# Performance work log

Hardware: AMD Instinct MI355X
Metric: run time of the kernel (lower is better)

Reference implementation:

```python
import jax, jax.numpy as jnp
import numpy as np

G = 512  # number of graphs per batch


def gcn_conv(x, edge_index, edge_attr, W):
    # x:[N,Fin], edge_index:[2,E], edge_attr:[E,1], W:[Fin,Fout]
    n = x.shape[0]
    loop = jnp.arange(n)
    row = jnp.concatenate([edge_index[0], loop])
    col = jnp.concatenate([edge_index[1], loop])
    w = jnp.concatenate([edge_attr[:, 0], jnp.ones((n,), x.dtype)])
    deg = jnp.zeros((n,), x.dtype).at[col].add(jnp.ones_like(w))
    dinv = jnp.clip(deg, 1e-12) ** -0.5
    norm = dinv[row] * w * dinv[col]
    h = x @ W  # [N,Fout]
    msg = h[row] * norm[:, None]  # [E+N,Fout] gather+scale
    return jnp.zeros_like(h).at[col].add(msg)  # scatter-add


def mean_pool(x, batch):
    s = jnp.zeros((G, x.shape[1]), x.dtype).at[batch].add(x)
    c = jnp.zeros((G,), x.dtype).at[batch].add(1.0)
    return s / jnp.clip(c, 1.0)[:, None]


def setup_inputs() -> dict:
    key = jax.random.key(0)
    ks = jax.random.split(key, 32)
    Nd, Ed, Np, Ep = 100000, 500000, 200000, 2000000
    d = {
        "drug_x": jax.random.normal(ks[0], (Nd, 78), jnp.float32),
        "drug_edge_index": jax.random.randint(ks[1], (2, Ed), 0, Nd),
        "drug_edge_attr": jax.random.uniform(ks[2], (Ed, 1), jnp.float32),
        "drug_batch": jnp.sort(jax.random.randint(ks[3], (Nd,), 0, G)),
        "protein_x": jax.random.normal(ks[4], (Np, 20), jnp.float32),
        "protein_edge_index": jax.random.randint(ks[5], (2, Ep), 0, Np),
        "protein_edge_attr": jax.random.uniform(ks[6], (Ep, 1), jnp.float32),
        "protein_batch": jnp.sort(jax.random.randint(ks[7], (Np,), 0, G)),
    }
    def w(k, i, o):
        return jax.random.normal(k, (i, o), jnp.float32) / np.sqrt(i)
    d.update({
        "dW1": w(ks[8], 78, 78), "dW2": w(ks[9], 78, 156), "dW3": w(ks[10], 156, 312),
        "dL1_w": w(ks[11], 312, 1024), "dL1_b": jnp.zeros((1024,), jnp.float32),
        "dL2_w": w(ks[12], 1024, 64), "dL2_b": jnp.zeros((64,), jnp.float32),
        "pW1": w(ks[13], 20, 20), "pW2": w(ks[14], 20, 40), "pW3": w(ks[15], 40, 80),
        "pL1_w": w(ks[16], 80, 1024), "pL1_b": jnp.zeros((1024,), jnp.float32),
        "pL2_w": w(ks[17], 1024, 64), "pL2_b": jnp.zeros((64,), jnp.float32),
        "fW1": w(ks[18], 128, 1024), "fb1": jnp.zeros((1024,), jnp.float32),
        "fW2": w(ks[19], 1024, 512), "fb2": jnp.zeros((512,), jnp.float32),
        "fW3": w(ks[20], 512, 1), "fb3": jnp.zeros((1,), jnp.float32),
    })
    return d


def reference(drug_x, drug_edge_index, drug_edge_attr, drug_batch,
              protein_x, protein_edge_index, protein_edge_attr, protein_batch,
              dW1, dW2, dW3, dL1_w, dL1_b, dL2_w, dL2_b,
              pW1, pW2, pW3, pL1_w, pL1_b, pL2_w, pL2_b,
              fW1, fb1, fW2, fb2, fW3, fb3):
    relu = jax.nn.relu
    x = relu(gcn_conv(drug_x, drug_edge_index, drug_edge_attr, dW1))
    x = relu(gcn_conv(x, drug_edge_index, drug_edge_attr, dW2))
    x = relu(gcn_conv(x, drug_edge_index, drug_edge_attr, dW3))
    x = mean_pool(x, drug_batch)
    x = relu(x @ dL1_w + dL1_b)
    x = relu(x @ dL2_w + dL2_b)
    p = relu(gcn_conv(protein_x, protein_edge_index, protein_edge_attr, pW1))
    p = relu(gcn_conv(p, protein_edge_index, protein_edge_attr, pW2))
    p = relu(gcn_conv(p, protein_edge_index, protein_edge_attr, pW3))
    p = mean_pool(p, protein_batch)
    p = relu(p @ pL1_w + pL1_b)
    p = relu(p @ pL2_w + pL2_b)
    c = jnp.concatenate([x, p], axis=1)  # [G,128]
    h = relu(c @ fW1 + fb1)
    h = relu(h @ fW2 + fb2)
    out = h @ fW3 + fb3  # [G,1]
    return out[:, 0]
```

## Files before the change

kernel.cpp:

```cpp
#include <hip/hip_runtime.h>
#include <math.h>

#define NGRAPH 512

typedef __attribute__((ext_vector_type(8))) __bf16 bf16x8;
typedef __attribute__((ext_vector_type(4))) float f32x4;

__device__ __forceinline__ unsigned short f2bf(float x) {
    unsigned int u = __float_as_uint(x);
    u = (u + 0x7fffu + ((u >> 16) & 1u)) >> 16;
    return (unsigned short)u;
}
__device__ __forceinline__ float bf2f(unsigned short b) {
    return __uint_as_float(((unsigned int)b) << 16);
}

static inline unsigned grid_for(size_t n, int block = 256) {
    return (unsigned)((n + block - 1) / block);
}

__global__ void fill_i32(int* __restrict__ p, int v, size_t n) {
    size_t i = blockIdx.x * (size_t)blockDim.x + threadIdx.x;
    if (i < n) p[i] = v;
}

__global__ void fill_f32(float* __restrict__ p, float v, size_t n) {
    size_t i = blockIdx.x * (size_t)blockDim.x + threadIdx.x;
    if (i < n) p[i] = v;
}

__global__ void hist_kernel(const int* __restrict__ col, int E, int* __restrict__ cnt) {
    size_t i = blockIdx.x * (size_t)blockDim.x + threadIdx.x;
    if (i < (size_t)E) atomicAdd(&cnt[col[i]], 1);
}

__global__ void wcvt_t(const float* __restrict__ in, unsigned short* __restrict__ out,
                       int K, int N, int KPAD) {
    int i = blockIdx.x * blockDim.x + threadIdx.x;
    if (i >= N * KPAD) return;
    int n = i / KPAD, k = i - n * KPAD;
    out[i] = (k < K) ? f2bf(in[(size_t)k * N + n]) : (unsigned short)0;
}

__global__ void scan_pass1(const int* __restrict__ in, int* __restrict__ bsum,
                           float* __restrict__ dinv, int n) {
    __shared__ int sdata[256];
    int tid = threadIdx.x;
    int i = blockIdx.x * 256 + tid;
    int v = (i < n) ? in[i] : 0;
    if (i < n) dinv[i] = 1.0f / sqrtf((float)v + 1.0f);
    sdata[tid] = v;
    __syncthreads();
    for (int s = 128; s > 0; s >>= 1) {
        if (tid < s) sdata[tid] += sdata[tid + s];
        __syncthreads();
    }
    if (tid == 0) bsum[blockIdx.x] = sdata[0];
}

__global__ void scan_pass2(int* __restrict__ bsum, int nb) {
    __shared__ int s[1024];
    int tid = threadIdx.x;
    int v = (tid < nb) ? bsum[tid] : 0;
    s[tid] = v;
    __syncthreads();
    for (int ofs = 1; ofs < 1024; ofs <<= 1) {
        int t = (tid >= ofs) ? s[tid - ofs] : 0;
        __syncthreads();
        s[tid] += t;
        __syncthreads();
    }
    if (tid < nb) bsum[tid] = s[tid] - v;
}

__global__ void scan_pass3(int* __restrict__ pos, const int* __restrict__ bsum, int n) {
    __shared__ int sdata[256];
    int tid = threadIdx.x;
    int i = blockIdx.x * 256 + tid;
    int v = (i < n) ? pos[i] : 0;
    sdata[tid] = v;
    __syncthreads();
    for (int ofs = 1; ofs < 256; ofs <<= 1) {
        int t = (tid >= ofs) ? sdata[tid - ofs] : 0;
        __syncthreads();
        sdata[tid] += t;
        __syncthreads();
    }
    if (i < n) pos[i] = sdata[tid] - v + bsum[blockIdx.x];
}

__global__ void csr_fill(const int* __restrict__ row, const int* __restrict__ col,
                         const float* __restrict__ attr, const float* __restrict__ dinv,
                         int* __restrict__ pos, int2* __restrict__ rcp, int E) {
    size_t i = blockIdx.x * (size_t)blockDim.x + threadIdx.x;
    if (i >= (size_t)E) return;
    int r = row[i], c = col[i];
    int slot = atomicAdd(&pos[c], 1);
    rcp[slot] = make_int2(r, __float_as_int(dinv[r] * attr[i] * dinv[c]));
}

template <int V, int LPG, int F, int LDI, int LDO, bool INBF>
__global__ void gather_bf(const int* __restrict__ pos, const int2* __restrict__ rcp,
                          const void* __restrict__ Xv, const float* __restrict__ dinv,
                          unsigned short* __restrict__ AGG, int N) {
    constexpr int gpb = 256 / LPG;
    int grp = threadIdx.x / LPG;
    if (grp >= gpb) return;
    int gid = blockIdx.x * gpb + grp;
    int lane = threadIdx.x - grp * LPG;
    if (gid >= N) return;

    auto load_row = [&](int r, float* dst) {
        if (INBF) {
            const unsigned short* X = (const unsigned short*)Xv;
            if (V == 2) {
                unsigned int u = *reinterpret_cast<const unsigned int*>(X + (size_t)r * LDI + lane * 2);
                dst[0] = bf2f((unsigned short)(u & 0xffffu));
                dst[1] = bf2f((unsigned short)(u >> 16));
            } else {
                uint2 u = *reinterpret_cast<const uint2*>(X + (size_t)r * LDI + lane * 4);
                dst[0] = bf2f((unsigned short)(u.x & 0xffffu));
                dst[1] = bf2f((unsigned short)(u.x >> 16));
                dst[2] = bf2f((unsigned short)(u.y & 0xffffu));
                dst[3] = bf2f((unsigned short)(u.y >> 16));
            }
        } else {
            const float* X = (const float*)Xv;
            if (V == 2) {
                float2 u = *reinterpret_cast<const float2*>(X + (size_t)r * LDI + lane * 2);
                dst[0] = u.x; dst[1] = u.y;
            } else {
                float4 u = *reinterpret_cast<const float4*>(X + (size_t)r * LDI + lane * 4);
                dst[0] = u.x; dst[1] = u.y; dst[2] = u.z; dst[3] = u.w;
            }
        }
    };

    int start = (gid == 0) ? 0 : pos[gid - 1];
    int end = pos[gid];
    float s = dinv[gid];
    float s2 = s * s;
    float acc[V];
    load_row(gid, acc);
#pragma unroll
    for (int j = 0; j < V; ++j) acc[j] *= s2;
    int t = start;
    for (; t + 4 <= end; t += 4) {
        int2 e0 = rcp[t], e1 = rcp[t + 1], e2 = rcp[t + 2], e3 = rcp[t + 3];
        float c0 = __int_as_float(e0.y), c1 = __int_as_float(e1.y);
        float c2 = __int_as_float(e2.y), c3 = __int_as_float(e3.y);
        float h0[V], h1[V], h2[V], h3[V];
        load_row(e0.x, h0); load_row(e1.x, h1); load_row(e2.x, h2); load_row(e3.x, h3);
#pragma unroll
        for (int j = 0; j < V; ++j) {
            float v = fmaf(c0, h0[j], acc[j]);
            v = fmaf(c1, h1[j], v);
            v = fmaf(c2, h2[j], v);
            acc[j] = fmaf(c3, h3[j], v);
        }
    }
    for (; t < end; ++t) {
        int2 e = rcp[t];
        float cf = __int_as_float(e.y);
        float h[V];
        load_row(e.x, h);
#pragma unroll
        for (int j = 0; j < V; ++j) acc[j] = fmaf(cf, h[j], acc[j]);
    }
    unsigned short* op = AGG + (size_t)gid * LDO + lane * V;
    if (V == 2) {
        unsigned int p = (unsigned int)f2bf(acc[0]) | ((unsigned int)f2bf(acc[1]) << 16);
        *reinterpret_cast<unsigned int*>(op) = p;
    } else {
        uint2 p;
        p.x = (unsigned int)f2bf(acc[0]) | ((unsigned int)f2bf(acc[1]) << 16);
        p.y = (unsigned int)f2bf(acc[2]) | ((unsigned int)f2bf(acc[3]) << 16);
        *reinterpret_cast<uint2*>(op) = p;
    }
    constexpr int PAD = LDO - F;
#pragma unroll
    for (int p = lane; p < PAD; p += LPG) AGG[(size_t)gid * LDO + F + p] = 0;
}

template <int KPAD, int BN>
__global__ __launch_bounds__(256) void tgemm_mfma(
        const unsigned short* __restrict__ A, const unsigned short* __restrict__ Wt,
        unsigned short* __restrict__ C, int M, int N, int ldc) {
    constexpr int CH = KPAD / 8;
    constexpr int KSTEPS = KPAD / 32;
    constexpr int NI = (BN / 2) / 16;
    __shared__ unsigned short As[128 * KPAD];
    const int tid = threadIdx.x;
    const int m0 = blockIdx.y * 128;
    const int n0 = blockIdx.x * BN;

    for (int idx = tid; idx < 128 * CH; idx += 256) {
        int m = idx / CH;
        int c = idx - m * CH;
        int gm = m0 + m;
        uint4 v = make_uint4(0u, 0u, 0u, 0u);
        if (gm < M) v = *reinterpret_cast<const uint4*>(A + (size_t)gm * KPAD + c * 8);
        int cs = c ^ (m & 7);
        *reinterpret_cast<uint4*>(&As[m * KPAD + cs * 8]) = v;
    }
    __syncthreads();

    const int wid = tid >> 6;
    const int l = tid & 63;
    const int wm = wid >> 1, wn = wid & 1;
    const int lr = l & 15, lg = l >> 4;

    f32x4 acc[4][NI];
#pragma unroll
    for (int i = 0; i < 4; ++i)
#pragma unroll
        for (int j = 0; j < NI; ++j) acc[i][j] = (f32x4){0.f, 0.f, 0.f, 0.f};

    for (int ks = 0; ks < KSTEPS; ++ks) {
        bf16x8 a[4], b[NI];
#pragma unroll
        for (int mi = 0; mi < 4; ++mi) {
            int row = wm * 64 + mi * 16 + lr;
            int cs = (ks * 4 + lg) ^ (row & 7);
            a[mi] = *reinterpret_cast<const bf16x8*>(&As[row * KPAD + cs * 8]);
        }
#pragma unroll
        for (int ni = 0; ni < NI; ++ni) {
            int gn = n0 + wn * (BN / 2) + ni * 16 + lr;
            int gns = (gn < N) ? gn : (N - 1);
            b[ni] = *reinterpret_cast<const bf16x8*>(
                &Wt[(size_t)gns * KPAD + ks * 32 + lg * 8]);
        }
#pragma unroll
        for (int mi = 0; mi < 4; ++mi)
#pragma unroll
            for (int ni = 0; ni < NI; ++ni)
                acc[mi][ni] = __builtin_amdgcn_mfma_f32_16x16x32_bf16(
                    a[mi], b[ni], acc[mi][ni], 0, 0, 0);
    }

#pragma unroll
    for (int mi = 0; mi < 4; ++mi) {
#pragma unroll
        for (int ni = 0; ni < NI; ++ni) {
#pragma unroll
            for (int j = 0; j < 4; ++j) {
                int gm = m0 + wm * 64 + mi * 16 + lg * 4 + j;
                int gn = n0 + wn * (BN / 2) + ni * 16 + lr;
                if (gm < M && gn < N)
                    C[(size_t)gm * ldc + gn] = f2bf(fmaxf(acc[mi][ni][j], 0.0f));
            }
        }
    }
}

template <int F2, int SUB>
__global__ void pool_part_bf(const unsigned short* __restrict__ X, const int* __restrict__ batch,
                             float* __restrict__ pool, int N, int PB) {
    int g = blockIdx.x / PB;
    int st = blockIdx.x - g * PB;
    int tid = threadIdx.x;
    int p = tid % F2;
    int sub = tid / F2;
    if (sub >= SUB) return;
    int lo = 0, hi = N;
    while (lo < hi) { int mid = (lo + hi) >> 1; if (batch[mid] < g) lo = mid + 1; else hi = mid; }
    int s0 = lo;
    hi = N;
    while (lo < hi) { int mid = (lo + hi) >> 1; if (batch[mid] < g + 1) lo = mid + 1; else hi = mid; }
    int s1 = lo;
    const int F = 2 * F2;
    int stride = PB * SUB;
    float a0 = 0.0f, a1 = 0.0f;
    for (int n = s0 + st * SUB + sub; n < s1; n += stride) {
        unsigned int u = *reinterpret_cast<const unsigned int*>(X + (size_t)n * F + 2 * p);
        a0 += fmaxf(bf2f((unsigned short)(u & 0xffffu)), 0.0f);
        a1 += fmaxf(bf2f((unsigned short)(u >> 16)), 0.0f);
    }
    atomicAdd(&pool[(size_t)g * F + 2 * p], a0);
    atomicAdd(&pool[(size_t)g * F + 2 * p + 1], a1);
}

__global__ void pool_div_g(float* __restrict__ pool, const int* __restrict__ batch,
                           int N, int F) {
    int g = blockIdx.x;
    int lo = 0, hi = N;
    while (lo < hi) { int mid = (lo + hi) >> 1; if (batch[mid] < g) lo = mid + 1; else hi = mid; }
    int s0 = lo;
    hi = N;
    while (lo < hi) { int mid = (lo + hi) >> 1; if (batch[mid] < g + 1) lo = mid + 1; else hi = mid; }
    int c = lo - s0;
    float inv = 1.0f / (float)(c > 0 ? c : 1);
    for (int f = threadIdx.x; f < F; f += blockDim.x)
        pool[(size_t)g * F + f] *= inv;
}

template <int K, int NOUT, bool INBF>
__global__ __launch_bounds__(64 * (K / 4)) void fused_conv_bf(
        const int* __restrict__ pos, const int2* __restrict__ rcp,
        const void* __restrict__ Xv, const float* __restrict__ dinv,
        const float* __restrict__ W, unsigned short* __restrict__ Y, int N) {
    constexpr int LPG = K / 4;
    constexpr int NTHREADS = 64 * LPG;
    __shared__ float Ws[K][NOUT];
    __shared__ float Ag[64][K + 8];
    const int tid = threadIdx.x;
    const int nid0 = blockIdx.x * 64;

    for (int i = tid; i < K * NOUT; i += NTHREADS) Ws[i / NOUT][i % NOUT] = W[i];

    int grp = tid / LPG, lane = tid % LPG;
    int gid = nid0 + grp;

    auto load_row = [&](int r, float* dst) {
        if (INBF) {
            const unsigned short* X = (const unsigned short*)Xv;
            uint2 u = *reinterpret_cast<const uint2*>(X + (size_t)r * K + lane * 4);
            dst[0] = bf2f((unsigned short)(u.x & 0xffffu));
            dst[1] = bf2f((unsigned short)(u.x >> 16));
            dst[2] = bf2f((unsigned short)(u.y & 0xffffu));
            dst[3] = bf2f((unsigned short)(u.y >> 16));
        } else {
            const float* X = (const float*)Xv;
            float4 u = *reinterpret_cast<const float4*>(X + (size_t)r * K + lane * 4);
            dst[0] = u.x; dst[1] = u.y; dst[2] = u.z; dst[3] = u.w;
        }
    };

    if (gid < N) {
        int start = (gid == 0) ? 0 : pos[gid - 1];
        int end = pos[gid];
        float s = dinv[gid];
        float s2 = s * s;
        float acc[4];
        load_row(gid, acc);
#pragma unroll
        for (int j = 0; j < 4; ++j) acc[j] *= s2;
        int t = start;
        for (; t + 4 <= end; t += 4) {
            int2 e0 = rcp[t], e1 = rcp[t + 1], e2 = rcp[t + 2], e3 = rcp[t + 3];
            float c0 = __int_as_float(e0.y), c1 = __int_as_float(e1.y);
            float c2 = __int_as_float(e2.y), c3 = __int_as_float(e3.y);
            float h0[4], h1[4], h2[4], h3[4];
            load_row(e0.x, h0); load_row(e1.x, h1); load_row(e2.x, h2); load_row(e3.x, h3);
#pragma unroll
            for (int j = 0; j < 4; ++j) {
                float v = fmaf(c0, h0[j], acc[j]);
                v = fmaf(c1, h1[j], v);
                v = fmaf(c2, h2[j], v);
                acc[j] = fmaf(c3, h3[j], v);
            }
        }
        for (; t < end; ++t) {
            int2 e = rcp[t];
            float cf = __int_as_float(e.y);
            float h[4];
            load_row(e.x, h);
#pragma unroll
            for (int j = 0; j < 4; ++j) acc[j] = fmaf(cf, h[j], acc[j]);
        }
#pragma unroll
        for (int j = 0; j < 4; ++j) Ag[grp][lane * 4 + j] = acc[j];
    }
    __syncthreads();

    for (int idx = tid; idx < 64 * NOUT; idx += NTHREADS) {
        int nl = idx / NOUT, n = idx % NOUT;
        int g = nid0 + nl;
        if (g < N) {
            float acc = 0.0f;
#pragma unroll
            for (int k = 0; k < K; ++k) acc = fmaf(Ag[nl][k], Ws[k][n], acc);
            Y[(size_t)g * NOUT + n] = f2bf(fmaxf(acc, 0.0f));
        }
    }
}

template <bool RELU_OUT>
__global__ __launch_bounds__(256) void skinny_gemm4(
        const float* __restrict__ A, const float* __restrict__ W,
        const float* __restrict__ bias, float* __restrict__ C,
        int K, int M, int ldc, int coff) {
    __shared__ float As[4][1024];
    __shared__ float red[4][64][4];
    const int tid = threadIdx.x;
    const int m_l = tid & 63;
    const int q = tid >> 6;
    const int g0 = blockIdx.y * 4;
    const int m0 = blockIdx.x * 64;

    for (int idx = tid; idx < 4 * K; idx += 256)
        As[idx / K][idx % K] = A[(size_t)(g0 + idx / K) * K + idx % K];
    __syncthreads();

    const int Kq = (K + 3) >> 2;
    const int ks = q * Kq;
    const int ke = (ks + Kq < K) ? ks + Kq : K;
    const int m = m0 + m_l;
    float acc[4] = {0.0f, 0.0f, 0.0f, 0.0f};
    if (m < M) {
        for (int k = ks; k < ke; ++k) {
            float w = W[(size_t)k * M + m];
            acc[0] = fmaf(As[0][k], w, acc[0]);
            acc[1] = fmaf(As[1][k], w, acc[1]);
            acc[2] = fmaf(As[2][k], w, acc[2]);
            acc[3] = fmaf(As[3][k], w, acc[3]);
        }
    }
#pragma unroll
    for (int g = 0; g < 4; ++g) red[q][m_l][g] = acc[g];
    __syncthreads();
    if (q == 0 && m < M) {
        float b = bias[m];
#pragma unroll
        for (int g = 0; g < 4; ++g) {
            float v = red[0][m_l][g] + red[1][m_l][g] + red[2][m_l][g] + red[3][m_l][g] + b;
            if (RELU_OUT) v = fmaxf(v, 0.0f);
            C[(size_t)(g0 + g) * ldc + coff + m] = v;
        }
    }
}

__global__ void final_kernel(const float* __restrict__ A, const float* __restrict__ w,
                             const float* __restrict__ b, float* __restrict__ out, int K) {
    int wave = (blockIdx.x * blockDim.x + threadIdx.x) >> 6;
    int lane = threadIdx.x & 63;
    if (wave >= NGRAPH) return;
    const float* ar = A + (size_t)wave * K;
    float acc = 0.0f;
    for (int k = lane; k < K; k += 64) acc = fmaf(ar[k], w[k], acc);
#pragma unroll
    for (int s = 32; s > 0; s >>= 1) acc += __shfl_down(acc, s, 64);
    if (lane == 0) out[wave] = acc + b[0];
}

static void build_csr(const int* row, const int* col, const float* attr,
                      int N, int E, float* dinv, int* pos,
                      int2* rcp, int* bsum, hipStream_t stream) {
    const int B = 256;
    int nb = (N + 255) / 256;
    fill_i32<<<grid_for(N), B, 0, stream>>>(pos, 0, (size_t)N);
    hist_kernel<<<grid_for(E), B, 0, stream>>>(col, E, pos);
    scan_pass1<<<nb, B, 0, stream>>>(pos, bsum, dinv, N);
    scan_pass2<<<1, 1024, 0, stream>>>(bsum, nb);
    scan_pass3<<<nb, B, 0, stream>>>(pos, bsum, N);
    csr_fill<<<grid_for(E), B, 0, stream>>>(row, col, attr, dinv, pos, rcp, E);
}

extern "C" void kernel_launch(void* const* d_in, const int* in_sizes, int n_in,
                              void* d_out, int out_size, void* d_ws, size_t ws_size,
                              hipStream_t stream) {
    const float* drug_x  = (const float*)d_in[0];
    const int*   d_ei    = (const int*)d_in[1];
    const float* d_ea    = (const float*)d_in[2];
    const int*   d_batch = (const int*)d_in[3];
    const float* prot_x  = (const float*)d_in[4];
    const int*   p_ei    = (const int*)d_in[5];
    const float* p_ea    = (const float*)d_in[6];
    const int*   p_batch = (const int*)d_in[7];
    const float* dW1 = (const float*)d_in[8];
    const float* dW2 = (const float*)d_in[9];
    const float* dW3 = (const float*)d_in[10];
    const float* dL1_w = (const float*)d_in[11];
    const float* dL1_b = (const float*)d_in[12];
    const float* dL2_w = (const float*)d_in[13];
    const float* dL2_b = (const float*)d_in[14];
    const float* pW1 = (const float*)d_in[15];
    const float* pW2 = (const float*)d_in[16];
    const float* pW3 = (const float*)d_in[17];
    const float* pL1_w = (const float*)d_in[18];
    const float* pL1_b = (const float*)d_in[19];
    const float* pL2_w = (const float*)d_in[20];
    const float* pL2_b = (const float*)d_in[21];
    const float* fW1 = (const float*)d_in[22];
    const float* fb1 = (const float*)d_in[23];
    const float* fW2 = (const float*)d_in[24];
    const float* fb2 = (const float*)d_in[25];
    const float* fW3 = (const float*)d_in[26];
    const float* fb3 = (const float*)d_in[27];
    float* out = (float*)d_out;

    const int Nd = in_sizes[0] / 78;
    const int Ed = in_sizes[1] / 2;
    const int Np = in_sizes[4] / 20;
    const int Ep = in_sizes[5] / 2;
    const int* d_row = d_ei;
    const int* d_col = d_ei + Ed;
    const int* p_row = p_ei;
    const int* p_col = p_ei + Ep;

    float* ws = (float*)d_ws;
    size_t off = 0;
    auto align256 = [](size_t n) -> size_t { return (n + 255) & ~(size_t)255; };
    auto take = [&](size_t n) -> float* {
        float* p = ws + off;
        off += align256(n);
        return p;
    };
    float* B1      = take((size_t)Nd * 312);
    float* B2      = take((size_t)Nd * 312);
    float* dinv_d  = take((size_t)Nd);
    float* dinv_p  = take((size_t)Np);
    float* pool    = take((size_t)NGRAPH * 312);
    float* t1      = take((size_t)NGRAPH * 1024);
    float* Cbuf    = take((size_t)NGRAPH * 128);
    float* f2buf   = take((size_t)NGRAPH * 512);
    int*   bsum    = (int*)take(1056);
    int*   pos_d   = (int*)take((size_t)Nd);
    int2*  rcp_d   = (int2*)take((size_t)Ed * 2);
    unsigned short* Wt1 = (unsigned short*)take((78 * 128) / 2);
    unsigned short* Wt2 = (unsigned short*)take((156 * 128) / 2);
    unsigned short* Wt3 = (unsigned short*)take((312 * 192) / 2);
    size_t tail = align256((size_t)Np * 80);
    int*   pos_p   = (int*)(B1 + tail);
    int2*  rcp_p   = (int2*)(B1 + tail + align256((size_t)Np));
    (void)ws_size;

    unsigned short* B1u = (unsigned short*)B1;
    unsigned short* B2u = (unsigned short*)B2;

    const int B = 256;
    auto gblocks = [](int n, int gpb) -> unsigned { return (unsigned)((n + gpb - 1) / gpb); };
    auto mgrid = [](int M, int N, int BN) -> dim3 {
        return dim3((unsigned)((N + BN - 1) / BN), (unsigned)((M + 127) / 128));
    };

    build_csr(d_row, d_col, d_ea, Nd, Ed, dinv_d, pos_d, rcp_d, bsum, stream);
    wcvt_t<<<grid_for(78 * 128), B, 0, stream>>>(dW1, Wt1, 78, 78, 128);
    wcvt_t<<<grid_for(156 * 128), B, 0, stream>>>(dW2, Wt2, 78, 156, 128);
    wcvt_t<<<grid_for(312 * 192), B, 0, stream>>>(dW3, Wt3, 156, 312, 192);

    gather_bf<2, 39, 78, 78, 128, false><<<gblocks(Nd, 256 / 39), B, 0, stream>>>(
        pos_d, rcp_d, drug_x, dinv_d, B2u, Nd);
    tgemm_mfma<128, 64><<<mgrid(Nd, 78, 64), B, 0, stream>>>(B2u, Wt1, B1u, Nd, 78, 80);

    gather_bf<2, 39, 78, 80, 128, true><<<gblocks(Nd, 256 / 39), B, 0, stream>>>(
        pos_d, rcp_d, B1u, dinv_d, B2u, Nd);
    tgemm_mfma<128, 64><<<mgrid(Nd, 156, 64), B, 0, stream>>>(B2u, Wt2, B1u, Nd, 156, 156);

    gather_bf<4, 39, 156, 156, 192, true><<<gblocks(Nd, 256 / 39), B, 0, stream>>>(
        pos_d, rcp_d, B1u, dinv_d, B2u, Nd);
    tgemm_mfma<192, 64><<<mgrid(Nd, 312, 64), B, 0, stream>>>(B2u, Wt3, B1u, Nd, 312, 312);

    fill_f32<<<grid_for((size_t)NGRAPH * 312), B, 0, stream>>>(pool, 0.0f, (size_t)NGRAPH * 312);
    pool_part_bf<156, 1><<<NGRAPH * 8, B, 0, stream>>>(B1u, d_batch, pool, Nd, 8);
    pool_div_g<<<NGRAPH, B, 0, stream>>>(pool, d_batch, Nd, 312);

    skinny_gemm4<true><<<dim3(16, NGRAPH / 4), B, 0, stream>>>(pool, dL1_w, dL1_b, t1, 312, 1024, 1024, 0);
    skinny_gemm4<true><<<dim3(1, NGRAPH / 4), B, 0, stream>>>(t1, dL2_w, dL2_b, Cbuf, 1024, 64, 128, 0);

    build_csr(p_row, p_col, p_ea, Np, Ep, dinv_p, pos_p, rcp_p, bsum, stream);

    fused_conv_bf<20, 20, false><<<gblocks(Np, 64), 320, 0, stream>>>(
        pos_p, rcp_p, prot_x, dinv_p, pW1, B1u, Np);
    fused_conv_bf<20, 40, true><<<gblocks(Np, 64), 320, 0, stream>>>(
        pos_p, rcp_p, B1u, dinv_p, pW2, B2u, Np);
    fused_conv_bf<40, 80, true><<<gblocks(Np, 64), 640, 0, stream>>>(
        pos_p, rcp_p, B2u, dinv_p, pW3, B1u, Np);

    fill_f32<<<grid_for((size_t)NGRAPH * 80), B, 0, stream>>>(pool, 0.0f, (size_t)NGRAPH * 80);
    pool_part_bf<40, 6><<<NGRAPH * 8, B, 0, stream>>>(B1u, p_batch, pool, Np, 8);
    pool_div_g<<<NGRAPH, B, 0, stream>>>(pool, p_batch, Np, 80);

    skinny_gemm4<true><<<dim3(16, NGRAPH / 4), B, 0, stream>>>(pool, pL1_w, pL1_b, t1, 80, 1024, 1024, 0);
    skinny_gemm4<true><<<dim3(1, NGRAPH / 4), B, 0, stream>>>(t1, pL2_w, pL2_b, Cbuf, 1024, 64, 128, 64);

    skinny_gemm4<true><<<dim3(16, NGRAPH / 4), B, 0, stream>>>(Cbuf, fW1, fb1, t1, 128, 1024, 1024, 0);
    skinny_gemm4<true><<<dim3(8, NGRAPH / 4), B, 0, stream>>>(t1, fW2, fb2, f2buf, 1024, 512, 512, 0);
    final_kernel<<<grid_for((size_t)NGRAPH * 64), B, 0, stream>>>(f2buf, fW3, fb3, out, 512);
}
```

Measured before the change: 1.024 ms.

## Build CSR via two-level binning to localize atomics in shared memory

Result: slower. 1.563 ms (+52.7%).

```diff
diff --git a/kernel.cpp b/kernel.cpp
--- a/kernel.cpp
+++ b/kernel.cpp
@@ -87,16 +87,42 @@
         __syncthreads();
     }
     if (i < n) pos[i] = sdata[tid] - v + bsum[blockIdx.x];
-}
-
-__global__ void csr_fill(const int* __restrict__ row, const int* __restrict__ col,
+    if (i == n - 1) pos[n] = sdata[tid] + bsum[blockIdx.x];
+}
+
+__global__ void bump_init(const int* __restrict__ pos, int* __restrict__ bump, int NB, int SPB) {
+    int b = blockIdx.x * blockDim.x + threadIdx.x;
+    if (b < NB) bump[b] = pos[b * SPB];
+}
+
+__global__ void bin_fill(const int* __restrict__ row, const int* __restrict__ col,
                          const float* __restrict__ attr, const float* __restrict__ dinv,
-                         int* __restrict__ pos, int2* __restrict__ rcp, int E) {
+                         int* __restrict__ bump, int4* __restrict__ tmp, int E, int SPB) {
     size_t i = blockIdx.x * (size_t)blockDim.x + threadIdx.x;
     if (i >= (size_t)E) return;
     int r = row[i], c = col[i];
-    int slot = atomicAdd(&pos[c], 1);
-    rcp[slot] = make_int2(r, __float_as_int(dinv[r] * attr[i] * dinv[c]));
+    int slot = atomicAdd(&bump[c / SPB], 1);
+    tmp[slot] = make_int4(r, c, __float_as_int(dinv[r] * attr[i] * dinv[c]), 0);
+}
+
+template <int SPB>
+__global__ __launch_bounds__(256) void csr_place(const int* __restrict__ pos,
+                                                 const int4* __restrict__ tmp,
+                                                 int2* __restrict__ rcp, int N) {
+    __shared__ int bl[SPB];
+    int b = blockIdx.x;
+    int lo = b * SPB;
+    int hi = lo + SPB; if (hi > N) hi = N;
+    int nn = hi - lo;
+    for (int i = threadIdx.x; i < nn; i += 256) bl[i] = pos[lo + i];
+    __syncthreads();
+    int base = pos[lo];
+    int cnt = pos[hi] - base;
+    for (int idx = threadIdx.x; idx < cnt; idx += 256) {
+        int4 t = tmp[base + idx];
+        int ls = atomicAdd(&bl[t.y - lo], 1);
+        rcp[ls] = make_int2(t.x, t.z);
+    }
 }
 
 template <int V, int LPG, int F, int LDI, int LDO, bool INBF>
@@ -136,8 +162,8 @@
         }
     };
 
-    int start = (gid == 0) ? 0 : pos[gid - 1];
-    int end = pos[gid];
+    int start = pos[gid];
+    int end = pos[gid + 1];
     float s = dinv[gid];
     float s2 = s * s;
     float acc[V];
@@ -328,8 +354,8 @@
     };
 
     if (gid < N) {
-        int start = (gid == 0) ? 0 : pos[gid - 1];
-        int end = pos[gid];
+        int start = pos[gid];
+        int end = pos[gid + 1];
         float s = dinv[gid];
         float s2 = s * s;
         float acc[4];
@@ -435,16 +461,20 @@
 }
 
 static void build_csr(const int* row, const int* col, const float* attr,
-                      int N, int E, float* dinv, int* pos,
-                      int2* rcp, int* bsum, hipStream_t stream) {
+                      int N, int E, float* dinv, int* pos, int2* rcp,
+                      int* bsum, int* bump, int4* tmp, hipStream_t stream) {
     const int B = 256;
+    const int SPB = 256;
     int nb = (N + 255) / 256;
+    int NB = (N + SPB - 1) / SPB;
     fill_i32<<<grid_for(N), B, 0, stream>>>(pos, 0, (size_t)N);
     hist_kernel<<<grid_for(E), B, 0, stream>>>(col, E, pos);
     scan_pass1<<<nb, B, 0, stream>>>(pos, bsum, dinv, N);
     scan_pass2<<<1, 1024, 0, stream>>>(bsum, nb);
     scan_pass3<<<nb, B, 0, stream>>>(pos, bsum, N);
-    csr_fill<<<grid_for(E), B, 0, stream>>>(row, col, attr, dinv, pos, rcp, E);
+    bump_init<<<grid_for(NB), B, 0, stream>>>(pos, bump, NB, SPB);
+    bin_fill<<<grid_for(E), B, 0, stream>>>(row, col, attr, dinv, bump, tmp, E, SPB);
+    csr_place<256><<<NB, B, 0, stream>>>(pos, tmp, rcp, N);
 }
 
 extern "C" void kernel_launch(void* const* d_in, const int* in_sizes, int n_in,
@@ -506,14 +536,16 @@
     float* Cbuf    = take((size_t)NGRAPH * 128);
     float* f2buf   = take((size_t)NGRAPH * 512);
     int*   bsum    = (int*)take(1056);
-    int*   pos_d   = (int*)take((size_t)Nd);
+    int*   bump    = (int*)take(1024);
+    int*   pos_d   = (int*)take((size_t)Nd + 1);
     int2*  rcp_d   = (int2*)take((size_t)Ed * 2);
     unsigned short* Wt1 = (unsigned short*)take((78 * 128) / 2);
     unsigned short* Wt2 = (unsigned short*)take((156 * 128) / 2);
     unsigned short* Wt3 = (unsigned short*)take((312 * 192) / 2);
+    int4*  tmp     = (int4*)(B2 + align256((size_t)Nd * 96));
     size_t tail = align256((size_t)Np * 80);
     int*   pos_p   = (int*)(B1 + tail);
-    int2*  rcp_p   = (int2*)(B1 + tail + align256((size_t)Np));
+    int2*  rcp_p   = (int2*)(B1 + tail + align256((size_t)Np + 1));
     (void)ws_size;
 
     unsigned short* B1u = (unsigned short*)B1;
@@ -525,7 +557,7 @@
         return dim3((unsigned)((N + BN - 1) / BN), (unsigned)((M + 127) / 128));
     };
 
-    build_csr(d_row, d_col, d_ea, Nd, Ed, dinv_d, pos_d, rcp_d, bsum, stream);
+    build_csr(d_row, d_col, d_ea, Nd, Ed, dinv_d, pos_d, rcp_d, bsum, bump, tmp, stream);
     wcvt_t<<<grid_for(78 * 128), B, 0, stream>>>(dW1, Wt1, 78, 78, 128);
     wcvt_t<<<grid_for(156 * 128), B, 0, stream>>>(dW2, Wt2, 78, 156, 128);
     wcvt_t<<<grid_for(312 * 192), B, 0, stream>>>(dW3, Wt3, 156, 312, 192);
@@ -549,7 +581,7 @@
     skinny_gemm4<true><<<dim3(16, NGRAPH / 4), B, 0, stream>>>(pool, dL1_w, dL1_b, t1, 312, 1024, 1024, 0);
     skinny_gemm4<true><<<dim3(1, NGRAPH / 4), B, 0, stream>>>(t1, dL2_w, dL2_b, Cbuf, 1024, 64, 128, 0);
 
-    build_csr(p_row, p_col, p_ea, Np, Ep, dinv_p, pos_p, rcp_p, bsum, stream);
+    build_csr(p_row, p_col, p_ea, Np, Ep, dinv_p, pos_p, rcp_p, bsum, bump, tmp, stream);
 
     fused_conv_bf<20, 20, false><<<gblocks(Np, 64), 320, 0, stream>>>(
         pos_p, rcp_p, prot_x, dinv_p, pW1, B1u, Np);
```
